# Performance work log

Hardware: AMD Instinct MI355X
Metric: run time of the kernel (lower is better)

The kernel has to match this reference:

```python
import jax, jax.numpy as jnp
import numpy as np

ALPHA = 50.0
EPS = 1e-12  # torch F.normalize eps


def setup_inputs() -> dict:
    key = jax.random.key(0)
    k1, k2 = jax.random.split(key)
    N, C, H, W_sp, K = 64, 128, 64, 64, 64
    x = jax.random.normal(k1, (N, C, H, W_sp), dtype=jnp.float32)
    # centroids.permute(1,0): shape [C, K]; orthogonal-ish init approximated by scaled gaussian
    W = jax.random.normal(k2, (C, K), dtype=jnp.float32) * (1.0 / np.sqrt(C))
    bias = jnp.zeros((K,), dtype=jnp.float32)
    return {"x": x, "W": W, "bias": bias}


def _l2norm(v, axis):
    return v / jnp.maximum(jnp.linalg.norm(v, axis=axis, keepdims=True), EPS)


def reference(x, W, bias):
    N, C, H, W_sp = x.shape
    K = W.shape[1]
    x = _l2norm(x, axis=1)                      # normalize over channels
    xf = x.reshape(N, C, H * W_sp)              # [N, C, P]
    Wn = _l2norm(W, axis=0)                     # column-normalized weight [C, K]
    # soft assignment logits, computed directly in [N, K, P] layout
    sa_logits = jnp.einsum('ncp,ck->nkp', xf, Wn)
    sa = jax.nn.softmax((sa_logits + bias[None, :, None]) * ALPHA, axis=1)  # over clusters
    # VLAD via two GEMM-like contractions instead of the [N,K,C,P] residual tensor:
    # vlad[n,k,c] = sum_p sa[n,k,p] * xf[n,c,p] - W[c,k] * sum_p sa[n,k,p]
    vlad = jnp.einsum('nkp,ncp->nkc', sa, xf) - sa.sum(axis=-1)[:, :, None] * W.T[None]
    vlad = _l2norm(vlad, axis=2)                # intra-normalize per cluster
    vlad = vlad.reshape(N, K * C)
    vlad = _l2norm(vlad, axis=1)                # global L2
    return (vlad, sa_logits)                    # original returns soft_assign_ permuted to [N, K, P]
```

## Files before the change

kernel.cpp:

```cpp
#include <hip/hip_runtime.h>
#include <math.h>

#define ALPHA 50.0f
#define EPS 1e-12f

constexpr int N = 64, C = 128, P = 4096, K = 64;
constexpr int NCH2 = 8;

typedef short short8_t __attribute__((ext_vector_type(8)));
typedef short short4_t __attribute__((ext_vector_type(4)));
typedef float f4 __attribute__((ext_vector_type(4)));
typedef unsigned int u32x4 __attribute__((ext_vector_type(4)));
typedef unsigned int u32x2 __attribute__((ext_vector_type(2)));

__device__ __forceinline__ unsigned short f2bf(float f) {
    union { float f; unsigned u; } v; v.f = f;
    unsigned r = (v.u + 0x7FFFu + ((v.u >> 16) & 1u)) >> 16;
    return (unsigned short)r;
}

__device__ __forceinline__ unsigned cvtpk(float lo, float hi) {
    unsigned r;
    asm("v_cvt_pk_bf16_f32 %0, %1, %2" : "=v"(r) : "v"(lo), "v"(hi));
    return r;
}

__device__ __forceinline__ void bar_lds() {
    asm volatile("s_waitcnt lgkmcnt(0)" ::: "memory");
    __builtin_amdgcn_s_barrier();
}

__global__ __launch_bounds__(256, 2) void k_fused(
    const float* __restrict__ x, const float* __restrict__ W,
    const float* __restrict__ bias, float* __restrict__ logits,
    float* __restrict__ vlad_part, float* __restrict__ Spart,
    float* __restrict__ ss2acc)
{
    __shared__ __align__(16) char smem[47616];
    unsigned short* xsT  = (unsigned short*)smem;
    unsigned short* xsN  = (unsigned short*)(smem + 17408);
    unsigned short* sa2s = (unsigned short*)(smem + 36864);
    float*          biass= (float*)(smem + 46080);
    float*          Sb2  = (float*)(smem + 46336);
    float*          red  = Sb2;
    float*          cinv = (float*)(smem + 47360);
    float*          Wl   = (float*)smem;

    const int tid  = threadIdx.x;
    const int n    = blockIdx.x >> 3;
    const int blk8 = blockIdx.x & 7;
    const int pbase = blk8 * 512;

    const int w = tid >> 6, lane = tid & 63;
    const int q = lane >> 4, l15 = lane & 15;
    const int c2 = lane >> 2, px4 = lane & 3;

    if (blockIdx.x == 0 && tid < 64) ss2acc[tid] = 0.f;
    if (tid < K) biass[tid] = bias[tid] * ALPHA;

    const float* xw = x + (size_t)n * C * P + pbase + 16 * w + 4 * px4 + (size_t)(8 * c2) * P;
    float4 va[8];
    short8_t af[4][4];
    float bzv[16];

    {
        float4 wv[8];
        #pragma unroll
        for (int it = 0; it < 8; ++it)
            wv[it] = *(const float4*)&W[(size_t)(tid + it * 256) * 4];
        #pragma unroll
        for (int j = 0; j < 8; ++j) va[j] = *(const float4*)&xw[(size_t)j * P];
        #pragma unroll
        for (int it = 0; it < 8; ++it) {
            const int idx4 = tid + it * 256;
            *(float4*)&Wl[(idx4 >> 4) * 68 + (idx4 & 15) * 4] = wv[it];
        }
        bar_lds();
        {
            const int k = tid & 63, part = tid >> 6;
            float s = 0.f;
            #pragma unroll
            for (int i = 0; i < 32; ++i) {
                float v = Wl[(part * 32 + i) * 68 + k];
                s = fmaf(v, v, s);
            }
            red[tid] = s;
        }
        bar_lds();
        if (tid < 64)
            cinv[tid] = 1.0f / fmaxf(
                sqrtf(red[tid] + red[64 + tid] + red[128 + tid] + red[192 + tid]), EPS);
        bar_lds();
        #pragma unroll
        for (int kt = 0; kt < 4; ++kt) {
            const float cv = cinv[16 * kt + l15];
            #pragma unroll
            for (int s = 0; s < 4; ++s)
                #pragma unroll
                for (int j = 0; j < 8; ++j)
                    af[kt][s][j] = (short)f2bf(
                        Wl[(s * 32 + 8 * q + j) * 68 + 16 * kt + l15] * cv);
            #pragma unroll
            for (int r = 0; r < 4; ++r) bzv[4 * kt + r] = biass[16 * kt + 4 * q + r];
        }
        bar_lds();
    }

    f4 acc2[8];
    #pragma unroll
    for (int ct = 0; ct < 8; ++ct) acc2[ct] = (f4){0.f, 0.f, 0.f, 0.f};
    float Sreg[16];
    #pragma unroll
    for (int i = 0; i < 16; ++i) Sreg[i] = 0.f;

    unsigned short* xsTw = xsT + w * 2176;

    for (int ch = 0; ch < 8; ++ch) {
        const float* vf = (const float*)va;

        float pss[4] = {0.f, 0.f, 0.f, 0.f};
        #pragma unroll
        for (int j = 0; j < 8; ++j)
            #pragma unroll
            for (int i = 0; i < 4; ++i)
                pss[i] = fmaf(vf[j * 4 + i], vf[j * 4 + i], pss[i]);
        #pragma unroll
        for (int i = 0; i < 4; ++i) {
            pss[i] += __shfl_xor(pss[i], 4);
            pss[i] += __shfl_xor(pss[i], 8);
            pss[i] += __shfl_xor(pss[i], 16);
            pss[i] += __shfl_xor(pss[i], 32);
        }
        float iv4[4];
        #pragma unroll
        for (int i = 0; i < 4; ++i) iv4[i] = 1.0f / fmaxf(sqrtf(pss[i]), EPS);

        #pragma unroll
        for (int i = 0; i < 4; ++i) {
            u32x4 t;
            #pragma unroll
            for (int jj = 0; jj < 4; ++jj)
                t[jj] = cvtpk(vf[(2 * jj) * 4 + i], vf[(2 * jj + 1) * 4 + i]);
            const int row = 4 * px4 + i;
            *(u32x4*)&xsTw[row * 136 + 8 * (c2 ^ (row & 7))] = t;
        }
        #pragma unroll
        for (int j = 0; j < 8; ++j) {
            u32x2 t2;
            t2[0] = cvtpk(vf[j * 4 + 0], vf[j * 4 + 1]);
            t2[1] = cvtpk(vf[j * 4 + 2], vf[j * 4 + 3]);
            *(u32x2*)&xsN[(8 * c2 + j) * 76 + 16 * w + 4 * px4] = t2;
        }
        if (ch < 7) {
            #pragma unroll
            for (int j = 0; j < 8; ++j)
                va[j] = *(const float4*)&xw[(size_t)j * P + (ch + 1) * 64];
        }
        asm volatile("s_waitcnt lgkmcnt(0)" ::: "memory");
        __builtin_amdgcn_sched_barrier(0);

        f4 acc1[4];
        #pragma unroll
        for (int t = 0; t < 4; ++t) acc1[t] = (f4){0.f, 0.f, 0.f, 0.f};
        __builtin_amdgcn_s_setprio(1);
        #pragma unroll
        for (int s = 0; s < 4; ++s) {
            short8_t bf = *(const short8_t*)&xsTw[l15 * 136 + 8 * ((4 * s + q) ^ (l15 & 7))];
            #pragma unroll
            for (int kt = 0; kt < 4; ++kt)
                acc1[kt] = __builtin_amdgcn_mfma_f32_16x16x32_bf16(af[kt][s], bf, acc1[kt], 0, 0, 0);
        }
        __builtin_amdgcn_s_setprio(0);

        const float s0 = __shfl(iv4[0], l15 >> 2);
        const float s1 = __shfl(iv4[1], l15 >> 2);
        const float s2 = __shfl(iv4[2], l15 >> 2);
        const float s3 = __shfl(iv4[3], l15 >> 2);
        const int li = l15 & 3;
        const float myiv = (li == 0) ? s0 : (li == 1) ? s1 : (li == 2) ? s2 : s3;

        float* lgp = logits + (size_t)n * K * P + pbase + ch * 64 + 16 * w + l15;
        float ev[16];
        float dl = 0.f;
        #pragma unroll
        for (int kt = 0; kt < 4; ++kt)
            #pragma unroll
            for (int r = 0; r < 4; ++r) {
                const float lv = acc1[kt][r] * myiv;
                __builtin_nontemporal_store(lv, &lgp[(size_t)(16 * kt + 4 * q + r) * P]);
                const float e = __expf(fmaf(lv, ALPHA, bzv[4 * kt + r]));
                ev[4 * kt + r] = e;
                dl += e;
            }
        dl += __shfl_xor(dl, 16);
        dl += __shfl_xor(dl, 32);
        const float rf = 1.0f / dl;
        const float sc = rf * myiv;
        #pragma unroll
        for (int kt = 0; kt < 4; ++kt)
            #pragma unroll
            for (int r = 0; r < 4; ++r) {
                const float e = ev[4 * kt + r];
                Sreg[4 * kt + r] += e * rf;
                sa2s[(16 * kt + 4 * q + r) * 72 + 16 * w + l15] = f2bf(e * sc);
            }
        bar_lds();

        {
            short8_t a2[2];
            #pragma unroll
            for (int kit = 0; kit < 2; ++kit)
                a2[kit] = *(const short8_t*)&sa2s[(16 * w + l15) * 72 + kit * 32 + 8 * q];
            __builtin_amdgcn_s_setprio(1);
            #pragma unroll
            for (int ct = 0; ct < 8; ++ct)
                #pragma unroll
                for (int kit = 0; kit < 2; ++kit) {
                    const unsigned short* bp = &xsN[(ct * 16 + l15) * 76 + kit * 32 + 8 * q];
                    short4_t b0 = *(const short4_t*)bp;
                    short4_t b1 = *(const short4_t*)(bp + 4);
                    short8_t bb;
                    bb[0] = b0[0]; bb[1] = b0[1]; bb[2] = b0[2]; bb[3] = b0[3];
                    bb[4] = b1[0]; bb[5] = b1[1]; bb[6] = b1[2]; bb[7] = b1[3];
                    acc2[ct] = __builtin_amdgcn_mfma_f32_16x16x32_bf16(a2[kit], bb, acc2[ct], 0, 0, 0);
                }
            __builtin_amdgcn_s_setprio(0);
        }
        bar_lds();
    }

    float* vp = vlad_part + ((size_t)blk8 * N + n) * (size_t)(K * C);
    #pragma unroll
    for (int ct = 0; ct < 8; ++ct)
        #pragma unroll
        for (int r = 0; r < 4; ++r)
            vp[(16 * w + 4 * q + r) * C + ct * 16 + l15] = acc2[ct][r];

    #pragma unroll
    for (int i = 0; i < 16; ++i) {
        Sreg[i] += __shfl_xor(Sreg[i], 1);
        Sreg[i] += __shfl_xor(Sreg[i], 2);
        Sreg[i] += __shfl_xor(Sreg[i], 4);
        Sreg[i] += __shfl_xor(Sreg[i], 8);
    }
    if (l15 == 0) {
        #pragma unroll
        for (int i = 0; i < 16; ++i)
            Sb2[w * 64 + 16 * (i >> 2) + 4 * q + (i & 3)] = Sreg[i];
    }
    __syncthreads();
    if (tid < 64)
        Spart[((size_t)blk8 * N + n) * K + tid] =
            Sb2[tid] + Sb2[64 + tid] + Sb2[128 + tid] + Sb2[192 + tid];
}

__global__ __launch_bounds__(256) void k_post1(
    const float* __restrict__ vlad_part, const float* __restrict__ W,
    const float* __restrict__ Spart, float* __restrict__ out,
    float* __restrict__ ss2acc)
{
    __shared__ float red[8];
    const int tid = threadIdx.x;
    const int n  = blockIdx.x >> 3;
    const int kq = blockIdx.x & 7;
    const int kl = tid >> 5;
    const int ci = tid & 31;
    const int k  = kq * 8 + kl;
    const int c0 = ci * 4;

    float Sk = 0.f;
    #pragma unroll
    for (int ch = 0; ch < NCH2; ++ch) Sk += Spart[(size_t)(ch * N + n) * K + k];

    float v[4];
    #pragma unroll
    for (int l = 0; l < 4; ++l) v[l] = 0.f;
    #pragma unroll
    for (int ch = 0; ch < NCH2; ++ch) {
        const float* vp = vlad_part + ((size_t)(ch * N + n) * K + k) * C + c0;
        float4 a = *(const float4*)&vp[0];
        v[0] += a.x; v[1] += a.y; v[2] += a.z; v[3] += a.w;
    }

    float ss = 0.f;
    #pragma unroll
    for (int l = 0; l < 4; ++l) {
        float val = v[l] - W[(size_t)(c0 + l) * K + k] * Sk;
        v[l] = val;
        ss = fmaf(val, val, ss);
    }
    ss += __shfl_xor(ss, 1);
    ss += __shfl_xor(ss, 2);
    ss += __shfl_xor(ss, 4);
    ss += __shfl_xor(ss, 8);
    ss += __shfl_xor(ss, 16);
    const float inv1 = 1.0f / fmaxf(sqrtf(ss), EPS);
    float ss2 = 0.f;
    #pragma unroll
    for (int l = 0; l < 4; ++l) { v[l] *= inv1; ss2 = fmaf(v[l], v[l], ss2); }
    ss2 += __shfl_xor(ss2, 1);
    ss2 += __shfl_xor(ss2, 2);
    ss2 += __shfl_xor(ss2, 4);
    ss2 += __shfl_xor(ss2, 8);
    ss2 += __shfl_xor(ss2, 16);
    if (ci == 0) red[kl] = ss2;
    __syncthreads();
    if (tid == 0) {
        float t = 0.f;
        #pragma unroll
        for (int i = 0; i < 8; ++i) t += red[i];
        atomicAdd(&ss2acc[n], t);
    }

    float* op = out + (size_t)n * K * C + (size_t)k * C + c0;
    *(float4*)&op[0] = (float4){v[0], v[1], v[2], v[3]};
}

__global__ __launch_bounds__(256) void k_post2(
    float* __restrict__ out, const float* __restrict__ ss2acc)
{
    const int n   = blockIdx.x >> 2;
    const int seg = blockIdx.x & 3;
    const float inv2 = 1.0f / fmaxf(sqrtf(ss2acc[n]), EPS);
    float* p = out + (size_t)n * K * C + (size_t)seg * 2048 + (size_t)threadIdx.x * 8;
    float4 a = *(const float4*)&p[0];
    float4 b = *(const float4*)&p[4];
    a.x *= inv2; a.y *= inv2; a.z *= inv2; a.w *= inv2;
    b.x *= inv2; b.y *= inv2; b.z *= inv2; b.w *= inv2;
    *(float4*)&p[0] = a;
    *(float4*)&p[4] = b;
}

extern "C" void kernel_launch(void* const* d_in, const int* in_sizes, int n_in,
                              void* d_out, int out_size, void* d_ws, size_t ws_size,
                              hipStream_t stream)
{
    const float* x    = (const float*)d_in[0];
    const float* W    = (const float*)d_in[1];
    const float* bias = (const float*)d_in[2];

    float* out_vlad   = (float*)d_out;
    float* out_logits = (float*)d_out + (size_t)N * K * C;

    float* ss2acc     = (float*)((char*)d_ws + 16384);
    float* Spart      = (float*)((char*)d_ws + 32768);
    float* vlad_part  = (float*)((char*)d_ws + 32768 + 131072);

    k_fused<<<dim3(N * NCH2), dim3(256), 0, stream>>>(
        x, W, bias, out_logits, vlad_part, Spart, ss2acc);
    k_post1<<<dim3(N * 8), dim3(256), 0, stream>>>(vlad_part, W, Spart, out_vlad, ss2acc);
    k_post2<<<dim3(N * 4), dim3(256), 0, stream>>>(out_vlad, ss2acc);
}
```

Measured before the change: 236.1 us.

## Precompute normalized weights, double-buffer x loads, stage logits through LDS

Adds a single-block prep kernel that column-normalizes W once and writes a bf16 transposed copy, so each fused block loads its MFMA fragments directly instead of redoing the normalization per block. The fused loop now keeps two register buffers of x and prefetches two chunks ahead, giving global loads more time to arrive. Logits are written to an LDS tile and then stored as coalesced float4 rows instead of scattered scalar nontemporal stores. The costs are an extra tiny launch, more registers for the second prefetch buffer, and more LDS (64.5KB), which may limit the two-blocks-per-CU occupancy target.

After: 273.6 us. 1.16x slower.

```diff
diff --git a/kernel.cpp b/kernel.cpp
--- a/kernel.cpp
+++ b/kernel.cpp
@@ -30,21 +30,52 @@
     __builtin_amdgcn_s_barrier();
 }
 
+__global__ __launch_bounds__(256) void k_prep(
+    const float* __restrict__ W, unsigned short* __restrict__ wnT,
+    float* __restrict__ ss2acc)
+{
+    __shared__ float Wl[C * 65];
+    __shared__ float red[256];
+    __shared__ float cinv[K];
+    const int tid = threadIdx.x;
+    if (tid < K) ss2acc[tid] = 0.f;
+    for (int idx = tid; idx < C * K; idx += 256) {
+        int c = idx >> 6, k = idx & 63;
+        Wl[c * 65 + k] = W[idx];
+    }
+    __syncthreads();
+    {
+        const int k = tid & 63, part = tid >> 6;
+        float s = 0.f;
+        #pragma unroll
+        for (int i = 0; i < 32; ++i) {
+            float v = Wl[(part * 32 + i) * 65 + k];
+            s = fmaf(v, v, s);
+        }
+        red[tid] = s;
+    }
+    __syncthreads();
+    if (tid < K)
+        cinv[tid] = 1.0f / fmaxf(
+            sqrtf(red[tid] + red[64 + tid] + red[128 + tid] + red[192 + tid]), EPS);
+    __syncthreads();
+    for (int idx = tid; idx < K * C; idx += 256) {
+        int k = idx >> 7, c = idx & 127;
+        wnT[idx] = f2bf(Wl[c * 65 + k] * cinv[k]);
+    }
+}
+
 __global__ __launch_bounds__(256, 2) void k_fused(
-    const float* __restrict__ x, const float* __restrict__ W,
+    const float* __restrict__ x, const unsigned short* __restrict__ wnT,
     const float* __restrict__ bias, float* __restrict__ logits,
-    float* __restrict__ vlad_part, float* __restrict__ Spart,
-    float* __restrict__ ss2acc)
-{
-    __shared__ __align__(16) char smem[47616];
+    float* __restrict__ vlad_part, float* __restrict__ Spart)
+{
+    __shared__ __align__(16) char smem[64512];
     unsigned short* xsT  = (unsigned short*)smem;
     unsigned short* xsN  = (unsigned short*)(smem + 17408);
     unsigned short* sa2s = (unsigned short*)(smem + 36864);
-    float*          biass= (float*)(smem + 46080);
-    float*          Sb2  = (float*)(smem + 46336);
-    float*          red  = Sb2;
-    float*          cinv = (float*)(smem + 47360);
-    float*          Wl   = (float*)smem;
+    float*          lgs  = (float*)(smem + 46080);
+    float*          Sb2  = (float*)(smem + 63488);
 
     const int tid  = threadIdx.x;
     const int n    = blockIdx.x >> 3;
@@ -55,55 +86,23 @@
     const int q = lane >> 4, l15 = lane & 15;
     const int c2 = lane >> 2, px4 = lane & 3;
 
-    if (blockIdx.x == 0 && tid < 64) ss2acc[tid] = 0.f;
-    if (tid < K) biass[tid] = bias[tid] * ALPHA;
-
     const float* xw = x + (size_t)n * C * P + pbase + 16 * w + 4 * px4 + (size_t)(8 * c2) * P;
-    float4 va[8];
+    float4 vA[8], vB[8];
     short8_t af[4][4];
     float bzv[16];
 
-    {
-        float4 wv[8];
-        #pragma unroll
-        for (int it = 0; it < 8; ++it)
-            wv[it] = *(const float4*)&W[(size_t)(tid + it * 256) * 4];
-        #pragma unroll
-        for (int j = 0; j < 8; ++j) va[j] = *(const float4*)&xw[(size_t)j * P];
-        #pragma unroll
-        for (int it = 0; it < 8; ++it) {
-            const int idx4 = tid + it * 256;
-            *(float4*)&Wl[(idx4 >> 4) * 68 + (idx4 & 15) * 4] = wv[it];
-        }
-        bar_lds();
-        {
-            const int k = tid & 63, part = tid >> 6;
-            float s = 0.f;
-            #pragma unroll
-            for (int i = 0; i < 32; ++i) {
-                float v = Wl[(part * 32 + i) * 68 + k];
-                s = fmaf(v, v, s);
-            }
-            red[tid] = s;
-        }
-        bar_lds();
-        if (tid < 64)
-            cinv[tid] = 1.0f / fmaxf(
-                sqrtf(red[tid] + red[64 + tid] + red[128 + tid] + red[192 + tid]), EPS);
-        bar_lds();
-        #pragma unroll
-        for (int kt = 0; kt < 4; ++kt) {
-            const float cv = cinv[16 * kt + l15];
-            #pragma unroll
-            for (int s = 0; s < 4; ++s)
-                #pragma unroll
-                for (int j = 0; j < 8; ++j)
-                    af[kt][s][j] = (short)f2bf(
-                        Wl[(s * 32 + 8 * q + j) * 68 + 16 * kt + l15] * cv);
-            #pragma unroll
-            for (int r = 0; r < 4; ++r) bzv[4 * kt + r] = biass[16 * kt + 4 * q + r];
-        }
-        bar_lds();
+    #pragma unroll
+    for (int j = 0; j < 8; ++j) vA[j] = *(const float4*)&xw[(size_t)j * P];
+    #pragma unroll
+    for (int j = 0; j < 8; ++j) vB[j] = *(const float4*)&xw[(size_t)j * P + 64];
+    #pragma unroll
+    for (int kt = 0; kt < 4; ++kt) {
+        #pragma unroll
+        for (int s = 0; s < 4; ++s)
+            af[kt][s] = *(const short8_t*)&wnT[(16 * kt + l15) * 128 + s * 32 + 8 * q];
+        #pragma unroll
+        for (int r = 0; r < 4; ++r)
+            bzv[4 * kt + r] = bias[16 * kt + 4 * q + r] * ALPHA;
     }
 
     f4 acc2[8];
@@ -115,118 +114,132 @@
 
     unsigned short* xsTw = xsT + w * 2176;
 
-    for (int ch = 0; ch < 8; ++ch) {
-        const float* vf = (const float*)va;
-
-        float pss[4] = {0.f, 0.f, 0.f, 0.f};
-        #pragma unroll
-        for (int j = 0; j < 8; ++j)
-            #pragma unroll
-            for (int i = 0; i < 4; ++i)
-                pss[i] = fmaf(vf[j * 4 + i], vf[j * 4 + i], pss[i]);
-        #pragma unroll
-        for (int i = 0; i < 4; ++i) {
-            pss[i] += __shfl_xor(pss[i], 4);
-            pss[i] += __shfl_xor(pss[i], 8);
-            pss[i] += __shfl_xor(pss[i], 16);
-            pss[i] += __shfl_xor(pss[i], 32);
+    for (int ch2 = 0; ch2 < 8; ch2 += 2) {
+        #pragma unroll
+        for (int ph = 0; ph < 2; ++ph) {
+            const int ch = ch2 + ph;
+            float4 (&vcur)[8] = ph ? vB : vA;
+            const float* vf = (const float*)vcur;
+
+            float pss[4] = {0.f, 0.f, 0.f, 0.f};
+            #pragma unroll
+            for (int j = 0; j < 8; ++j)
+                #pragma unroll
+                for (int i = 0; i < 4; ++i)
+                    pss[i] = fmaf(vf[j * 4 + i], vf[j * 4 + i], pss[i]);
+            #pragma unroll
+            for (int i = 0; i < 4; ++i) {
+                pss[i] += __shfl_xor(pss[i], 4);
+                pss[i] += __shfl_xor(pss[i], 8);
+                pss[i] += __shfl_xor(pss[i], 16);
+                pss[i] += __shfl_xor(pss[i], 32);
+            }
+            float iv4[4];
+            #pragma unroll
+            for (int i = 0; i < 4; ++i) iv4[i] = 1.0f / fmaxf(sqrtf(pss[i]), EPS);
+
+            #pragma unroll
+            for (int i = 0; i < 4; ++i) {
+                u32x4 t;
+                #pragma unroll
+                for (int jj = 0; jj < 4; ++jj)
+                    t[jj] = cvtpk(vf[(2 * jj) * 4 + i], vf[(2 * jj + 1) * 4 + i]);
+                const int row = 4 * px4 + i;
+                *(u32x4*)&xsTw[row * 136 + 8 * (c2 ^ (row & 7))] = t;
+            }
+            #pragma unroll
+            for (int j = 0; j < 8; ++j) {
+                u32x2 t2;
+                t2[0] = cvtpk(vf[j * 4 + 0], vf[j * 4 + 1]);
+                t2[1] = cvtpk(vf[j * 4 + 2], vf[j * 4 + 3]);
+                *(u32x2*)&xsN[(8 * c2 + j) * 76 + 16 * w + 4 * px4] = t2;
+            }
+            if (ch + 2 < 8) {
+                #pragma unroll
+                for (int j = 0; j < 8; ++j)
+                    vcur[j] = *(const float4*)&xw[(size_t)j * P + (ch + 2) * 64];
+            }
+            asm volatile("s_waitcnt lgkmcnt(0)" ::: "memory");
+            __builtin_amdgcn_sched_barrier(0);
+
+            f4 acc1[4];
+            #pragma unroll
+            for (int t = 0; t < 4; ++t) acc1[t] = (f4){0.f, 0.f, 0.f, 0.f};
+            __builtin_amdgcn_s_setprio(1);
+            #pragma unroll
+            for (int s = 0; s < 4; ++s) {
+                short8_t bf = *(const short8_t*)&xsTw[l15 * 136 + 8 * ((4 * s + q) ^ (l15 & 7))];
+                #pragma unroll
+                for (int kt = 0; kt < 4; ++kt)
+                    acc1[kt] = __builtin_amdgcn_mfma_f32_16x16x32_bf16(af[kt][s], bf, acc1[kt], 0, 0, 0);
+            }
+            __builtin_amdgcn_s_setprio(0);
+
+            const float s0 = __shfl(iv4[0], l15 >> 2);
+            const float s1 = __shfl(iv4[1], l15 >> 2);
+            const float s2 = __shfl(iv4[2], l15 >> 2);
+            const float s3 = __shfl(iv4[3], l15 >> 2);
+            const int li = l15 & 3;
+            const float myiv = (li == 0) ? s0 : (li == 1) ? s1 : (li == 2) ? s2 : s3;
+
+            float ev[16];
+            float dl = 0.f;
+            #pragma unroll
+            for (int kt = 0; kt < 4; ++kt)
+                #pragma unroll
+                for (int r = 0; r < 4; ++r) {
+                    const float lv = acc1[kt][r] * myiv;
+                    lgs[(16 * kt + 4 * q + r) * 68 + 16 * w + l15] = lv;
+                    const float e = __expf(fmaf(lv, ALPHA, bzv[4 * kt + r]));
+                    ev[4 * kt + r] = e;
+                    dl += e;
+                }
+            dl += __shfl_xor(dl, 16);
+            dl += __shfl_xor(dl, 32);
+            const float rf = 1.0f / dl;
+            const float sc = rf * myiv;
+            #pragma unroll
+            for (int kt = 0; kt < 4; ++kt)
+                #pragma unroll
+                for (int r = 0; r < 4; ++r) {
+                    const float e = ev[4 * kt + r];
+                    Sreg[4 * kt + r] += e * rf;
+                    sa2s[(16 * kt + 4 * q + r) * 72 + 16 * w + l15] = f2bf(e * sc);
+                }
+            bar_lds();
+
+            {
+                float* lgp = logits + (size_t)n * K * P + pbase + ch * 64;
+                #pragma unroll
+                for (int jj = 0; jj < 4; ++jj) {
+                    const int k = 16 * w + 4 * jj + (lane >> 4);
+                    const f4 t = *(const f4*)&lgs[k * 68 + 4 * (lane & 15)];
+                    *(f4*)&lgp[(size_t)k * P + 4 * (lane & 15)] = t;
+                }
+            }
+
+            {
+                short8_t a2[2];
+                #pragma unroll
+                for (int kit = 0; kit < 2; ++kit)
+                    a2[kit] = *(const short8_t*)&sa2s[(16 * w + l15) * 72 + kit * 32 + 8 * q];
+                __builtin_amdgcn_s_setprio(1);
+                #pragma unroll
+                for (int ct = 0; ct < 8; ++ct)
+                    #pragma unroll
+                    for (int kit = 0; kit < 2; ++kit) {
+                        const unsigned short* bp = &xsN[(ct * 16 + l15) * 76 + kit * 32 + 8 * q];
+                        short4_t b0 = *(const short4_t*)bp;
+                        short4_t b1 = *(const short4_t*)(bp + 4);
+                        short8_t bb;
+                        bb[0] = b0[0]; bb[1] = b0[1]; bb[2] = b0[2]; bb[3] = b0[3];
+                        bb[4] = b1[0]; bb[5] = b1[1]; bb[6] = b1[2]; bb[7] = b1[3];
+                        acc2[ct] = __builtin_amdgcn_mfma_f32_16x16x32_bf16(a2[kit], bb, acc2[ct], 0, 0, 0);
+                    }
+                __builtin_amdgcn_s_setprio(0);
+            }
+            bar_lds();
         }
-        float iv4[4];
-        #pragma unroll
-        for (int i = 0; i < 4; ++i) iv4[i] = 1.0f / fmaxf(sqrtf(pss[i]), EPS);
-
-        #pragma unroll
-        for (int i = 0; i < 4; ++i) {
-            u32x4 t;
-            #pragma unroll
-            for (int jj = 0; jj < 4; ++jj)
-                t[jj] = cvtpk(vf[(2 * jj) * 4 + i], vf[(2 * jj + 1) * 4 + i]);
-            const int row = 4 * px4 + i;
-            *(u32x4*)&xsTw[row * 136 + 8 * (c2 ^ (row & 7))] = t;
-        }
-        #pragma unroll
-        for (int j = 0; j < 8; ++j) {
-            u32x2 t2;
-            t2[0] = cvtpk(vf[j * 4 + 0], vf[j * 4 + 1]);
-            t2[1] = cvtpk(vf[j * 4 + 2], vf[j * 4 + 3]);
-            *(u32x2*)&xsN[(8 * c2 + j) * 76 + 16 * w + 4 * px4] = t2;
-        }
-        if (ch < 7) {
-            #pragma unroll
-            for (int j = 0; j < 8; ++j)
-                va[j] = *(const float4*)&xw[(size_t)j * P + (ch + 1) * 64];
-        }
-        asm volatile("s_waitcnt lgkmcnt(0)" ::: "memory");
-        __builtin_amdgcn_sched_barrier(0);
-
-        f4 acc1[4];
-        #pragma unroll
-        for (int t = 0; t < 4; ++t) acc1[t] = (f4){0.f, 0.f, 0.f, 0.f};
-        __builtin_amdgcn_s_setprio(1);
-        #pragma unroll
-        for (int s = 0; s < 4; ++s) {
-            short8_t bf = *(const short8_t*)&xsTw[l15 * 136 + 8 * ((4 * s + q) ^ (l15 & 7))];
-            #pragma unroll
-            for (int kt = 0; kt < 4; ++kt)
-                acc1[kt] = __builtin_amdgcn_mfma_f32_16x16x32_bf16(af[kt][s], bf, acc1[kt], 0, 0, 0);
-        }
-        __builtin_amdgcn_s_setprio(0);
-
-        const float s0 = __shfl(iv4[0], l15 >> 2);
-        const float s1 = __shfl(iv4[1], l15 >> 2);
-        const float s2 = __shfl(iv4[2], l15 >> 2);
-        const float s3 = __shfl(iv4[3], l15 >> 2);
-        const int li = l15 & 3;
-        const float myiv = (li == 0) ? s0 : (li == 1) ? s1 : (li == 2) ? s2 : s3;
-
-        float* lgp = logits + (size_t)n * K * P + pbase + ch * 64 + 16 * w + l15;
-        float ev[16];
-        float dl = 0.f;
-        #pragma unroll
-        for (int kt = 0; kt < 4; ++kt)
-            #pragma unroll
-            for (int r = 0; r < 4; ++r) {
-                const float lv = acc1[kt][r] * myiv;
-                __builtin_nontemporal_store(lv, &lgp[(size_t)(16 * kt + 4 * q + r) * P]);
-                const float e = __expf(fmaf(lv, ALPHA, bzv[4 * kt + r]));
-                ev[4 * kt + r] = e;
-                dl += e;
-            }
-        dl += __shfl_xor(dl, 16);
-        dl += __shfl_xor(dl, 32);
-        const float rf = 1.0f / dl;
-        const float sc = rf * myiv;
-        #pragma unroll
-        for (int kt = 0; kt < 4; ++kt)
-            #pragma unroll
-            for (int r = 0; r < 4; ++r) {
-                const float e = ev[4 * kt + r];
-                Sreg[4 * kt + r] += e * rf;
-                sa2s[(16 * kt + 4 * q + r) * 72 + 16 * w + l15] = f2bf(e * sc);
-            }
-        bar_lds();
-
-        {
-            short8_t a2[2];
-            #pragma unroll
-            for (int kit = 0; kit < 2; ++kit)
-                a2[kit] = *(const short8_t*)&sa2s[(16 * w + l15) * 72 + kit * 32 + 8 * q];
-            __builtin_amdgcn_s_setprio(1);
-            #pragma unroll
-            for (int ct = 0; ct < 8; ++ct)
-                #pragma unroll
-                for (int kit = 0; kit < 2; ++kit) {
-                    const unsigned short* bp = &xsN[(ct * 16 + l15) * 76 + kit * 32 + 8 * q];
-                    short4_t b0 = *(const short4_t*)bp;
-                    short4_t b1 = *(const short4_t*)(bp + 4);
-                    short8_t bb;
-                    bb[0] = b0[0]; bb[1] = b0[1]; bb[2] = b0[2]; bb[3] = b0[3];
-                    bb[4] = b1[0]; bb[5] = b1[1]; bb[6] = b1[2]; bb[7] = b1[3];
-                    acc2[ct] = __builtin_amdgcn_mfma_f32_16x16x32_bf16(a2[kit], bb, acc2[ct], 0, 0, 0);
-                }
-            __builtin_amdgcn_s_setprio(0);
-        }
-        bar_lds();
     }
 
     float* vp = vlad_part + ((size_t)blk8 * N + n) * (size_t)(K * C);
@@ -342,12 +355,14 @@
     float* out_vlad   = (float*)d_out;
     float* out_logits = (float*)d_out + (size_t)N * K * C;
 
-    float* ss2acc     = (float*)((char*)d_ws + 16384);
-    float* Spart      = (float*)((char*)d_ws + 32768);
-    float* vlad_part  = (float*)((char*)d_ws + 32768 + 131072);
-
+    unsigned short* wnT = (unsigned short*)d_ws;
+    float* ss2acc       = (float*)((char*)d_ws + 16384);
+    float* Spart        = (float*)((char*)d_ws + 32768);
+    float* vlad_part    = (float*)((char*)d_ws + 32768 + 131072);
+
+    k_prep<<<dim3(1), dim3(256), 0, stream>>>(W, wnT, ss2acc);
     k_fused<<<dim3(N * NCH2), dim3(256), 0, stream>>>(
-        x, W, bias, out_logits, vlad_part, Spart, ss2acc);
+        x, wnT, bias, out_logits, vlad_part, Spart);
     k_post1<<<dim3(N * 8), dim3(256), 0, stream>>>(vlad_part, W, Spart, out_vlad, ss2acc);
     k_post2<<<dim3(N * 4), dim3(256), 0, stream>>>(out_vlad, ss2acc);
 }
```
